# Optimization experiments

Hardware: AMD Instinct MI355X
Metric: run time of the kernel (lower is better)

Reference implementation:

```python
import jax, jax.numpy as jnp
import numpy as np

B = 32       # batch_size
N = 8192     # points per set
D = 128      # d_in
LAM = 0.01   # lambda_ ridge regularizer


def setup_inputs() -> dict:
    key = jax.random.key(0)
    x = jax.random.normal(key, (B, N, D), dtype=jnp.float32)
    return {"x": x}


def reference(x):
    Bb, Nn, Dd = x.shape
    # mean-center over the point dim, then batched cov = diffs^T @ diffs / (N-1)
    diffs = x - x.mean(axis=1, keepdims=True)                  # (B, N, D)
    cov = jnp.einsum('bnd,bne->bde', diffs, diffs) / (Nn - 1)  # (B, D, D)
    cov = cov + LAM * jnp.eye(Dd, dtype=x.dtype)
    # torch.unique(dim=1) with generic float data: rows are all distinct,
    # so it reduces to a lexicographic ascending sort of the D rows.
    # jnp.lexsort uses the LAST key as primary -> reverse columns of m.T.
    idx = jax.vmap(lambda m: jnp.lexsort(m.T[::-1]))(cov)      # (B, D)
    sorted_cov = jnp.take_along_axis(cov, idx[:, :, None], axis=1)
    return sorted_cov.reshape(Bb, Dd * Dd)                     # (B, d_out)
```

## Files before the change

### kernel.cpp

```cpp
#include <hip/hip_runtime.h>
#include <hip/hip_bf16.h>

#define DD 128
#define NPTS 8192
#define BBATCH 32
#define BK 64
#define LAM 0.01f

typedef __attribute__((ext_vector_type(8))) short bf16x8;
typedef __attribute__((ext_vector_type(16))) float f32x16;

__device__ __forceinline__ unsigned f2bf_u(float f) {
    unsigned u = __builtin_bit_cast(unsigned, f);
    return (u + 0x7FFFu + ((u >> 16) & 1u)) >> 16;
}
__device__ __forceinline__ float bf2f(unsigned short u) {
    unsigned v = ((unsigned)u) << 16;
    return __builtin_bit_cast(float, v);
}
__device__ __forceinline__ int swz(int d) { return ((d >> 2) ^ d) & 7; }

template<int P>
__global__ __launch_bounds__(512, 4) void gram_stats(
    const float* __restrict__ x, unsigned short* __restrict__ Spart,
    float* __restrict__ CSpart, float* __restrict__ KDpart)
{
    __shared__ short XT[2][DD * BK];
    constexpr int rowsPerBlk = NPTS / P;
    constexpr int T = rowsPerBlk / BK;

    const int blk = blockIdx.x;
    const int b   = blk & 31;
    const int kc  = blk >> 5;
    const int k0g = kc * rowsPerBlk;
    const float* xb = x + (size_t)b * NPTS * DD;

    const int tid    = threadIdx.x;
    const int lane   = tid & 63;
    const int wave   = tid >> 6;
    const int dg     = tid & 31;
    const int rowgrp = tid >> 5;
    const int chunk  = rowgrp >> 1;
    const int wr32   = (wave & 3) * 32;
    const int wc64   = (wave >> 2) * 64;

    f32x16 acc0 = {}; f32x16 acc1 = {};
    float csum[4] = {0.f, 0.f, 0.f, 0.f};
    float kdot[4] = {0.f, 0.f, 0.f, 0.f};
    float4 R0, R1, R2, R3;

    auto issueLoads = [&](int kt) {
        const float4* s = (const float4*)(xb + (size_t)(k0g + kt + rowgrp * 4) * DD) + dg;
        R0 = s[0]; R1 = s[32]; R2 = s[64]; R3 = s[96];
    };
    auto convertStore = [&](int buf) {
        float x00 = __shfl(R0.x, lane & 32);
        float x01 = __shfl(R1.x, lane & 32);
        float x02 = __shfl(R2.x, lane & 32);
        float x03 = __shfl(R3.x, lane & 32);
        float e0[4] = {R0.x, R0.y, R0.z, R0.w};
        float e1[4] = {R1.x, R1.y, R1.z, R1.w};
        float e2[4] = {R2.x, R2.y, R2.z, R2.w};
        float e3[4] = {R3.x, R3.y, R3.z, R3.w};
        short* Xb = XT[buf];
        #pragma unroll
        for (int i = 0; i < 4; ++i) {
            csum[i] += e0[i] + e1[i] + e2[i] + e3[i];
            kdot[i] += x00 * e0[i] + x01 * e1[i] + x02 * e2[i] + x03 * e3[i];
            const int d = 4 * dg + i;
            unsigned u0 = f2bf_u(e0[i]) | (f2bf_u(e1[i]) << 16);
            unsigned u1 = f2bf_u(e2[i]) | (f2bf_u(e3[i]) << 16);
            const int addr = d * BK + ((chunk ^ swz(d)) * 8) + (rowgrp & 1) * 4;
            uint2 v; v.x = u0; v.y = u1;
            *(uint2*)(Xb + addr) = v;
        }
    };

    issueLoads(0);
    convertStore(0);
    __syncthreads();

    for (int t = 0; t < T; ++t) {
        if (t + 1 < T) issueLoads((t + 1) * BK);
        const short* Xb = XT[t & 1];
        #pragma unroll
        for (int ks = 0; ks < BK / 16; ++ks) {
            const int cb = ks * 2 + (lane >> 5);
            const int m = lane & 31;
            const int ad = wr32 + m, b0d = wc64 + m, b1d = wc64 + 32 + m;
            bf16x8 a  = *(const bf16x8*)(Xb + ad  * BK + ((cb ^ swz(ad))  * 8));
            bf16x8 b0 = *(const bf16x8*)(Xb + b0d * BK + ((cb ^ swz(b0d)) * 8));
            bf16x8 b1 = *(const bf16x8*)(Xb + b1d * BK + ((cb ^ swz(b1d)) * 8));
            acc0 = __builtin_amdgcn_mfma_f32_32x32x16_bf16(a, b0, acc0, 0, 0, 0);
            acc1 = __builtin_amdgcn_mfma_f32_32x32x16_bf16(a, b1, acc1, 0, 0, 0);
        }
        if (t + 1 < T) convertStore((t + 1) & 1);
        __syncthreads();
    }

    unsigned short* Sp = Spart + ((size_t)b * P + kc) * (DD * DD);
    const int colLane = lane & 31;
    const int rowHw = 4 * (lane >> 5);
    #pragma unroll
    for (int r = 0; r < 16; ++r) {
        const int row = wr32 + (r & 3) + 8 * (r >> 2) + rowHw;
        Sp[row * DD + wc64 + colLane]      = (unsigned short)f2bf_u(acc0[r]);
        Sp[row * DD + wc64 + 32 + colLane] = (unsigned short)f2bf_u(acc1[r]);
    }

    __syncthreads();
    float* red = (float*)XT;
    #pragma unroll
    for (int i = 0; i < 4; ++i) {
        red[tid] = csum[i];
        __syncthreads();
        if (tid < 32) {
            float s = 0.f;
            #pragma unroll
            for (int g = 0; g < 16; ++g) s += red[g * 32 + tid];
            CSpart[((size_t)b * P + kc) * DD + 4 * tid + i] = s;
        }
        __syncthreads();
        red[tid] = kdot[i];
        __syncthreads();
        if (tid < 32) {
            float s = 0.f;
            #pragma unroll
            for (int g = 0; g < 16; ++g) s += red[g * 32 + tid];
            KDpart[((size_t)b * P + kc) * DD + 4 * tid + i] = s;
        }
        __syncthreads();
    }
}

template<int P>
__global__ __launch_bounds__(128) void keys_ranks(
    const float* __restrict__ CSpart, const float* __restrict__ KDpart,
    float* __restrict__ csOut, int* __restrict__ rankOut)
{
    __shared__ float csh[DD];
    __shared__ float key[DD];
    const int b = blockIdx.x;
    const int tid = threadIdx.x;
    float s = 0.f, kd = 0.f;
    #pragma unroll
    for (int p = 0; p < P; ++p) {
        s  += CSpart[((size_t)b * P + p) * DD + tid];
        kd += KDpart[((size_t)b * P + p) * DD + tid];
    }
    csh[tid] = s;
    __syncthreads();
    const float k = (kd - s * csh[0] * (1.f / NPTS)) * (1.f / (NPTS - 1))
                  + ((tid == 0) ? LAM : 0.f);
    key[tid] = k;
    __syncthreads();
    int r = 0;
    #pragma unroll 8
    for (int j = 0; j < DD; ++j) {
        const float kj = key[j];
        r += (kj < k) || (kj == k && j < tid);
    }
    csOut[b * DD + tid] = s;
    rankOut[b * DD + tid] = r;
}

template<int P>
__global__ __launch_bounds__(256) void reduce_scatter(
    const unsigned short* __restrict__ Spart, const float* __restrict__ csOut,
    const int* __restrict__ rankOut, float* __restrict__ out)
{
    __shared__ float csh[DD];
    __shared__ int rk[8];
    const int b = blockIdx.x;
    const int seg = blockIdx.y;
    const int tid = threadIdx.x;
    if (tid < DD) csh[tid] = csOut[b * DD + tid];
    if (tid < 8)  rk[tid] = rankOut[b * DD + seg * 8 + tid];

    const int base = seg * (8 * DD) + tid * 4;
    float a0 = 0.f, a1 = 0.f, a2 = 0.f, a3 = 0.f;
    #pragma unroll
    for (int p = 0; p < P; ++p) {
        uint2 v = *(const uint2*)(Spart + ((size_t)b * P + p) * (DD * DD) + base);
        a0 += bf2f((unsigned short)(v.x & 0xFFFFu));
        a1 += bf2f((unsigned short)(v.x >> 16));
        a2 += bf2f((unsigned short)(v.y & 0xFFFFu));
        a3 += bf2f((unsigned short)(v.y >> 16));
    }
    __syncthreads();
    const int row = seg * 8 + (tid >> 5);
    const int j0  = (tid & 31) * 4;
    const float ci = csh[row];
    const float invN = 1.f / NPTS, invNm1 = 1.f / (NPTS - 1);
    float4 v;
    v.x = (a0 - ci * csh[j0 + 0] * invN) * invNm1 + ((row == j0 + 0) ? LAM : 0.f);
    v.y = (a1 - ci * csh[j0 + 1] * invN) * invNm1 + ((row == j0 + 1) ? LAM : 0.f);
    v.z = (a2 - ci * csh[j0 + 2] * invN) * invNm1 + ((row == j0 + 2) ? LAM : 0.f);
    v.w = (a3 - ci * csh[j0 + 3] * invN) * invNm1 + ((row == j0 + 3) ? LAM : 0.f);
    float* o = out + (size_t)b * DD * DD + (size_t)rk[tid >> 5] * DD + j0;
    *(float4*)o = v;
}

template<int P>
static void launch_all(const float* x, float* out, void* d_ws, hipStream_t stream)
{
    size_t nS = (size_t)BBATCH * P * DD * DD;
    unsigned short* Spart = (unsigned short*)d_ws;
    float* CSpart = (float*)(Spart + nS);
    float* KDpart = CSpart + (size_t)BBATCH * P * DD;
    float* csOut  = KDpart + (size_t)BBATCH * P * DD;
    int*   rankOut = (int*)(csOut + (size_t)BBATCH * DD);

    gram_stats<P><<<dim3(32 * P), dim3(512), 0, stream>>>(x, Spart, CSpart, KDpart);
    keys_ranks<P><<<dim3(BBATCH), dim3(128), 0, stream>>>(CSpart, KDpart, csOut, rankOut);
    reduce_scatter<P><<<dim3(BBATCH, 16), dim3(256), 0, stream>>>(Spart, csOut, rankOut, out);
}

extern "C" void kernel_launch(void* const* d_in, const int* in_sizes, int n_in,
                              void* d_out, int out_size, void* d_ws, size_t ws_size,
                              hipStream_t stream)
{
    const float* x = (const float*)d_in[0];
    float* out = (float*)d_out;

    auto need = [](int P) {
        return (size_t)BBATCH * P * DD * DD * sizeof(unsigned short)
             + (size_t)BBATCH * P * 2 * DD * sizeof(float)
             + (size_t)BBATCH * DD * (sizeof(float) + sizeof(int));
    };
    if (need(16) <= ws_size)      launch_all<16>(x, out, d_ws, stream);
    else                          launch_all<8>(x, out, d_ws, stream);
}
```

Baseline: 198.4 us.

## Stream fp32 tiles to LDS via async global_load_lds with triple buffering

Replaces the register-staged global loads in the gram kernel with direct global-to-LDS DMA (global_load_lds), triple-buffered fp32 tiles prefetched two iterations ahead, with manual s_waitcnt and s_barrier sync. Threads then read fp32 from LDS, convert to bf16 into a double-buffered swizzled tile, and run MFMA. Shared memory grows to about 128KB and the occupancy hint is dropped, so far fewer blocks fit per CU. The split count also changes from 16 to 8 (4 as fallback), halving the partial Gram matrices written and reduced but exposing less parallelism.

```diff
diff --git a/kernel.cpp b/kernel.cpp
--- a/kernel.cpp
+++ b/kernel.cpp
@@ -20,20 +20,32 @@
 }
 __device__ __forceinline__ int swz(int d) { return ((d >> 2) ^ d) & 7; }
 
-template<int P>
-__global__ __launch_bounds__(512, 4) void gram_stats(
+#define ASM_BARRIER()  asm volatile("s_barrier" ::: "memory")
+#define WAIT_VM4()     asm volatile("s_waitcnt vmcnt(4)" ::: "memory")
+#define WAIT_VM0()     asm volatile("s_waitcnt vmcnt(0)" ::: "memory")
+#define WAIT_LGKM0()   asm volatile("s_waitcnt lgkmcnt(0)" ::: "memory")
+
+__device__ __forceinline__ void dma16(const void* g, void* l) {
+    __builtin_amdgcn_global_load_lds(
+        (const __attribute__((address_space(1))) void*)g,
+        (__attribute__((address_space(3))) void*)l, 16, 0, 0);
+}
+
+template<int P>
+__global__ __launch_bounds__(512) void gram_stats(
     const float* __restrict__ x, unsigned short* __restrict__ Spart,
     float* __restrict__ CSpart, float* __restrict__ KDpart)
 {
-    __shared__ short XT[2][DD * BK];
+    __shared__ char smem[3 * 32768 + 2 * 16384];
+    short* XT = (short*)(smem + 98304);
+
     constexpr int rowsPerBlk = NPTS / P;
     constexpr int T = rowsPerBlk / BK;
 
     const int blk = blockIdx.x;
     const int b   = blk & 31;
     const int kc  = blk >> 5;
-    const int k0g = kc * rowsPerBlk;
-    const float* xb = x + (size_t)b * NPTS * DD;
+    const float* xb = x + (size_t)b * NPTS * DD + (size_t)(kc * rowsPerBlk) * DD;
 
     const int tid    = threadIdx.x;
     const int lane   = tid & 63;
@@ -47,55 +59,63 @@
     f32x16 acc0 = {}; f32x16 acc1 = {};
     float csum[4] = {0.f, 0.f, 0.f, 0.f};
     float kdot[4] = {0.f, 0.f, 0.f, 0.f};
-    float4 R0, R1, R2, R3;
-
-    auto issueLoads = [&](int kt) {
-        const float4* s = (const float4*)(xb + (size_t)(k0g + kt + rowgrp * 4) * DD) + dg;
-        R0 = s[0]; R1 = s[32]; R2 = s[64]; R3 = s[96];
+
+    auto dmaTile = [&](int t) {
+        const char* g = (const char*)(xb + (size_t)t * BK * DD) + wave * 4096 + lane * 16;
+        char* l = smem + (t % 3) * 32768 + wave * 4096;
+        dma16(g,        l);
+        dma16(g + 1024, l + 1024);
+        dma16(g + 2048, l + 2048);
+        dma16(g + 3072, l + 3072);
     };
-    auto convertStore = [&](int buf) {
-        float x00 = __shfl(R0.x, lane & 32);
-        float x01 = __shfl(R1.x, lane & 32);
-        float x02 = __shfl(R2.x, lane & 32);
-        float x03 = __shfl(R3.x, lane & 32);
-        float e0[4] = {R0.x, R0.y, R0.z, R0.w};
-        float e1[4] = {R1.x, R1.y, R1.z, R1.w};
-        float e2[4] = {R2.x, R2.y, R2.z, R2.w};
-        float e3[4] = {R3.x, R3.y, R3.z, R3.w};
-        short* Xb = XT[buf];
+
+    dmaTile(0);
+    dmaTile(1);
+
+    for (int t = 0; t < T; ++t) {
+        if (t < T - 1) { WAIT_VM4(); } else { WAIT_VM0(); }
+        ASM_BARRIER();
+
+        const float* rw = (const float*)(smem + (t % 3) * 32768);
+        float4 R[4];
+        float xk[4];
+        #pragma unroll
+        for (int r = 0; r < 4; ++r) {
+            const int row = rowgrp * 4 + r;
+            R[r]  = *(const float4*)(rw + row * DD + dg * 4);
+            xk[r] = rw[row * DD];
+        }
+        short* Xb = XT + (t & 1) * 8192;
         #pragma unroll
         for (int i = 0; i < 4; ++i) {
-            csum[i] += e0[i] + e1[i] + e2[i] + e3[i];
-            kdot[i] += x00 * e0[i] + x01 * e1[i] + x02 * e2[i] + x03 * e3[i];
+            const float v0 = (&R[0].x)[i], v1 = (&R[1].x)[i];
+            const float v2 = (&R[2].x)[i], v3 = (&R[3].x)[i];
+            csum[i] += v0 + v1 + v2 + v3;
+            kdot[i] += xk[0] * v0 + xk[1] * v1 + xk[2] * v2 + xk[3] * v3;
             const int d = 4 * dg + i;
-            unsigned u0 = f2bf_u(e0[i]) | (f2bf_u(e1[i]) << 16);
-            unsigned u1 = f2bf_u(e2[i]) | (f2bf_u(e3[i]) << 16);
+            unsigned u0 = f2bf_u(v0) | (f2bf_u(v1) << 16);
+            unsigned u1 = f2bf_u(v2) | (f2bf_u(v3) << 16);
             const int addr = d * BK + ((chunk ^ swz(d)) * 8) + (rowgrp & 1) * 4;
-            uint2 v; v.x = u0; v.y = u1;
-            *(uint2*)(Xb + addr) = v;
-        }
-    };
-
-    issueLoads(0);
-    convertStore(0);
-    __syncthreads();
-
-    for (int t = 0; t < T; ++t) {
-        if (t + 1 < T) issueLoads((t + 1) * BK);
-        const short* Xb = XT[t & 1];
+            uint2 vv; vv.x = u0; vv.y = u1;
+            *(uint2*)(Xb + addr) = vv;
+        }
+        WAIT_LGKM0();
+        ASM_BARRIER();
+
+        if (t + 2 < T) dmaTile(t + 2);
+
+        const short* Xc = XT + (t & 1) * 8192;
         #pragma unroll
         for (int ks = 0; ks < BK / 16; ++ks) {
             const int cb = ks * 2 + (lane >> 5);
             const int m = lane & 31;
             const int ad = wr32 + m, b0d = wc64 + m, b1d = wc64 + 32 + m;
-            bf16x8 a  = *(const bf16x8*)(Xb + ad  * BK + ((cb ^ swz(ad))  * 8));
-            bf16x8 b0 = *(const bf16x8*)(Xb + b0d * BK + ((cb ^ swz(b0d)) * 8));
-            bf16x8 b1 = *(const bf16x8*)(Xb + b1d * BK + ((cb ^ swz(b1d)) * 8));
+            bf16x8 a  = *(const bf16x8*)(Xc + ad  * BK + ((cb ^ swz(ad))  * 8));
+            bf16x8 b0 = *(const bf16x8*)(Xc + b0d * BK + ((cb ^ swz(b0d)) * 8));
+            bf16x8 b1 = *(const bf16x8*)(Xc + b1d * BK + ((cb ^ swz(b1d)) * 8));
             acc0 = __builtin_amdgcn_mfma_f32_32x32x16_bf16(a, b0, acc0, 0, 0, 0);
             acc1 = __builtin_amdgcn_mfma_f32_32x32x16_bf16(a, b1, acc1, 0, 0, 0);
         }
-        if (t + 1 < T) convertStore((t + 1) & 1);
-        __syncthreads();
     }
 
     unsigned short* Sp = Spart + ((size_t)b * P + kc) * (DD * DD);
@@ -109,7 +129,7 @@
     }
 
     __syncthreads();
-    float* red = (float*)XT;
+    float* red = (float*)smem;
     #pragma unroll
     for (int i = 0; i < 4; ++i) {
         red[tid] = csum[i];
@@ -228,6 +248,6 @@
              + (size_t)BBATCH * P * 2 * DD * sizeof(float)
              + (size_t)BBATCH * DD * (sizeof(float) + sizeof(int));
     };
-    if (need(16) <= ws_size)      launch_all<16>(x, out, d_ws, stream);
-    else                          launch_all<8>(x, out, d_ws, stream);
-}
+    if (need(8) <= ws_size)       launch_all<8>(x, out, d_ws, stream);
+    else                          launch_all<4>(x, out, d_ws, stream);
+}
```

Result: no change. 202.3 us (+2.0%).
